# Performance work log

Hardware: AMD Instinct MI355X
Metric: run time of the kernel (lower is better)

## Reference

```python
import jax, jax.numpy as jnp
import numpy as np
import math

EMBED = 256
NH = 8            # num_heads
HD = EMBED // NH  # head_dim = 32
LEVELS = 4
P = 4             # points per level
SUMP = LEVELS * P # 16
OFFSET_SCALE = 0.5
SPATIAL = ((80, 80), (40, 40), (20, 20), (10, 10))  # (H, W) per level
BS, LQ = 4, 4096
LV = sum(h * w for h, w in SPATIAL)  # 8500


def _offset_bias():
    # replicates _reset_parameters grid init for sampling_offsets.bias
    thetas = np.arange(NH, dtype=np.float32) * (2.0 * math.pi / NH)
    grid = np.stack([np.cos(thetas), np.sin(thetas)], -1)  # [NH,2]
    grid = grid / np.abs(grid).max(-1, keepdims=True)
    grid = np.tile(grid.reshape(NH, 1, 2), (1, SUMP, 1))   # [NH,SUMP,2]
    scaling = np.concatenate([np.arange(1, P + 1) for _ in range(LEVELS)]).reshape(1, SUMP, 1)
    grid = grid * scaling
    return jnp.asarray(grid.reshape(-1), dtype=jnp.float32)  # [NH*SUMP*2]


def setup_inputs() -> dict:
    key = jax.random.key(0)
    ks = jax.random.split(key, 8)
    xavier = lambda k, fi, fo: jax.random.uniform(k, (fi, fo), jnp.float32,
                                                  -math.sqrt(6.0 / (fi + fo)), math.sqrt(6.0 / (fi + fo)))
    return {
        "query": jax.random.normal(ks[0], (BS, LQ, EMBED), jnp.float32),
        "reference_points": jax.random.uniform(ks[1], (BS, LQ, 1, 4), jnp.float32),
        "value": jax.random.normal(ks[2], (BS, LV, EMBED), jnp.float32),
        # sampling_offsets: weight is zero-init in torch; use small random so offsets depend on query
        "W_off": jax.random.normal(ks[3], (EMBED, NH * SUMP * 2), jnp.float32) * 0.01,
        "b_off": _offset_bias(),
        "W_attn": jax.random.normal(ks[4], (EMBED, NH * SUMP), jnp.float32) * 0.01,
        "b_attn": jnp.zeros((NH * SUMP,), jnp.float32),
        "W_v": xavier(ks[5], EMBED, EMBED),
        "b_v": jnp.zeros((EMBED,), jnp.float32),
        "W_o": xavier(ks[6], EMBED, EMBED),
        "b_o": jnp.zeros((EMBED,), jnp.float32),
    }


def _bilinear_sample(v_l, loc, Hl, Wl):
    """grid_sample (bilinear, zero padding, align_corners=False) on one level.
    v_l: [bs, NH, Hl*Wl, HD]; loc: [bs, Lq, NH, P, 2] in [0,1] (x=width, y=height).
    Returns [bs, Lq, NH, P, HD]."""
    bs, lq, nh, p, _ = loc.shape
    x = loc[..., 0] * Wl - 0.5
    y = loc[..., 1] * Hl - 0.5
    x0 = jnp.floor(x)
    y0 = jnp.floor(y)
    lx, ly = x - x0, y - y0
    x0i = x0.astype(jnp.int32)
    y0i = y0.astype(jnp.int32)

    def corner(xi, yi, w):
        valid = ((xi >= 0) & (xi < Wl) & (yi >= 0) & (yi < Hl)).astype(v_l.dtype)
        idx = jnp.clip(yi, 0, Hl - 1) * Wl + jnp.clip(xi, 0, Wl - 1)  # [bs,Lq,NH,P]
        idx = jnp.transpose(idx, (0, 2, 1, 3)).reshape(bs, nh, lq * p)
        g = jnp.take_along_axis(v_l, idx[..., None], axis=2)          # [bs,NH,Lq*P,HD]
        g = g.reshape(bs, nh, lq, p, HD).transpose(0, 2, 1, 3, 4)     # [bs,Lq,NH,P,HD]
        return g * (w * valid)[..., None]

    return (corner(x0i, y0i, (1 - lx) * (1 - ly))
            + corner(x0i + 1, y0i, lx * (1 - ly))
            + corner(x0i, y0i + 1, (1 - lx) * ly)
            + corner(x0i + 1, y0i + 1, lx * ly))


def reference(query, reference_points, value, W_off, b_off, W_attn, b_attn, W_v, b_v, W_o, b_o):
    bs, lq = query.shape[:2]
    lv = value.shape[1]

    v = (value @ W_v + b_v).reshape(bs, lv, NH, HD)

    off = (query @ W_off + b_off).reshape(bs, lq, NH, SUMP, 2)
    attn = jax.nn.softmax((query @ W_attn + b_attn).reshape(bs, lq, NH, SUMP), axis=-1)

    # reference_points last dim == 4 path (box refs)
    nps = jnp.full((SUMP, 1), 1.0 / P, dtype=query.dtype)  # num_points_scale
    loc = (reference_points[:, :, None, :, :2]
           + off * nps * reference_points[:, :, None, :, 2:] * OFFSET_SCALE)  # [bs,Lq,NH,SUMP,2]

    out = jnp.zeros((bs, lq, NH, HD), dtype=query.dtype)
    v_start, p_start = 0, 0
    for (Hl, Wl) in SPATIAL:
        n = Hl * Wl
        v_l = jnp.transpose(v[:, v_start:v_start + n], (0, 2, 1, 3))  # [bs,NH,n,HD]
        loc_l = loc[:, :, :, p_start:p_start + P]
        w_l = attn[:, :, :, p_start:p_start + P]
        sampled = _bilinear_sample(v_l, loc_l, Hl, Wl)                # [bs,Lq,NH,P,HD]
        out = out + jnp.einsum('blhpd,blhp->blhd', sampled, w_l)
        v_start += n
        p_start += P

    return out.reshape(bs, lq, EMBED) @ W_o + b_o
```

## Files before the change

### kernel.cpp

```cpp
#include <hip/hip_runtime.h>

#define NH 8
#define HD 32
#define SUMP 16
#define LQ 4096
#define BS 4
#define LV 8500
#define NQ (BS * LQ)
#define MV (BS * LV)

typedef float f32x4 __attribute__((ext_vector_type(4)));
typedef _Float16 f16x8 __attribute__((ext_vector_type(8)));

__global__ __launch_bounds__(256) void prep_kernel(
    const float* __restrict__ Wv, const float* __restrict__ Woff,
    const float* __restrict__ Wattn, const float* __restrict__ Wo,
    const float* __restrict__ boff, const float* __restrict__ battn,
    _Float16* __restrict__ WtVf, _Float16* __restrict__ WtOAf,
    _Float16* __restrict__ WtOf, float* __restrict__ biasOA)
{
    int g = blockIdx.x * 256 + threadIdx.x;
    int gl; _Float16* dst; int which;
    if (g < 65536)       { gl = g;          dst = WtVf;  which = 0; }
    else if (g < 163840) { gl = g - 65536;  dst = WtOAf; which = 1; }
    else                 { gl = g - 163840; dst = WtOf;  which = 2; }
    int e = gl & 7, m16 = (gl >> 3) & 15, q = (gl >> 7) & 3, C = (gl >> 9) & 7, T = gl >> 12;
    int n = T * 16 + m16, k = C * 32 + q * 8 + e;
    float w;
    if (which == 0)      w = Wv[k * 256 + n];
    else if (which == 1) w = (n < 256) ? Woff[k * 256 + n] : Wattn[k * 128 + (n - 256)];
    else                 w = Wo[k * 256 + n];
    dst[gl] = (_Float16)w;
    if (blockIdx.x == 0) biasOA[threadIdx.x] = boff[threadIdx.x];
    if (blockIdx.x == 1 && threadIdx.x < 128) biasOA[256 + threadIdx.x] = battn[threadIdx.x];
}

template <int NI, bool V_MODE, bool A_F16>
__device__ __forceinline__ void gemm_body(
    const float* __restrict__ A32, const _Float16* __restrict__ A16,
    const _Float16* __restrict__ Bf,
    const float* __restrict__ bias, void* __restrict__ Cv,
    int M, int N, int mb, int nb, _Float16* As )
{
    const int t = threadIdx.x;
    const int wave = t >> 6, lane = t & 63;
    const int quad = lane >> 4, l16 = lane & 15;
    const int mbase = mb * 128 + (wave & 1) * 64;
    const int ntile0 = nb * (2 * NI) + (wave >> 1) * NI;

    const int srow = t >> 2, skq = t & 3;
    int gm0 = mb * 128 + srow;        if (gm0 > M - 1) gm0 = M - 1;
    int gm1 = mb * 128 + srow + 64;   if (gm1 > M - 1) gm1 = M - 1;
    const float* ap0 = A32 ? A32 + (size_t)gm0 * 256 + skq * 8 : nullptr;
    const float* ap1 = A32 ? A32 + (size_t)gm1 * 256 + skq * 8 : nullptr;
    const _Float16* hp0 = A16 ? A16 + (size_t)gm0 * 256 + skq * 8 : nullptr;
    const _Float16* hp1 = A16 ? A16 + (size_t)gm1 * 256 + skq * 8 : nullptr;
    const int slot0 = (((srow >> 4)) * 64 + skq * 16 + ((srow & 15) ^ skq)) * 8;
    const int slot1 = ((((srow + 64) >> 4)) * 64 + skq * 16 + ((srow & 15) ^ skq)) * 8;

    const _Float16* bp[NI];
    #pragma unroll
    for (int ni = 0; ni < NI; ++ni)
        bp[ni] = Bf + (size_t)(ntile0 + ni) * 4096 + lane * 8;

    float a0[8], a1[8];
    f16x8 a0h, a1h;
    f16x8 bcur[NI], bnxt[NI];
    f32x4 acc[4][NI] = {};

    if (A_F16) {
        a0h = *(const f16x8*)(hp0);
        a1h = *(const f16x8*)(hp1);
    } else {
        *(float4*)(a0 + 0) = *(const float4*)(ap0 + 0);
        *(float4*)(a0 + 4) = *(const float4*)(ap0 + 4);
        *(float4*)(a1 + 0) = *(const float4*)(ap1 + 0);
        *(float4*)(a1 + 4) = *(const float4*)(ap1 + 4);
    }
    #pragma unroll
    for (int ni = 0; ni < NI; ++ni) bcur[ni] = *(const f16x8*)(bp[ni]);

    #pragma unroll
    for (int k = 0; k < 8; ++k) {
        _Float16* buf = As + (k & 1) * 4096;
        f16x8 c0, c1;
        if (A_F16) { c0 = a0h; c1 = a1h; }
        else {
            #pragma unroll
            for (int j = 0; j < 8; ++j) { c0[j] = (_Float16)a0[j]; c1[j] = (_Float16)a1[j]; }
        }
        *(f16x8*)(buf + slot0) = c0;
        *(f16x8*)(buf + slot1) = c1;
        __syncthreads();
        if (k < 7) {
            const int k0 = (k + 1) * 32;
            if (A_F16) {
                a0h = *(const f16x8*)(hp0 + k0);
                a1h = *(const f16x8*)(hp1 + k0);
            } else {
                *(float4*)(a0 + 0) = *(const float4*)(ap0 + k0);
                *(float4*)(a0 + 4) = *(const float4*)(ap0 + k0 + 4);
                *(float4*)(a1 + 0) = *(const float4*)(ap1 + k0);
                *(float4*)(a1 + 4) = *(const float4*)(ap1 + k0 + 4);
            }
            #pragma unroll
            for (int ni = 0; ni < NI; ++ni) bnxt[ni] = *(const f16x8*)(bp[ni] + (k + 1) * 512);
        }
        f16x8 af[4];
        #pragma unroll
        for (int mi = 0; mi < 4; ++mi)
            af[mi] = *(const f16x8*)(buf + (((wave & 1) * 4 + mi) * 64 + quad * 16 + (l16 ^ quad)) * 8);
        #pragma unroll
        for (int mi = 0; mi < 4; ++mi)
            #pragma unroll
            for (int ni = 0; ni < NI; ++ni)
                acc[mi][ni] = __builtin_amdgcn_mfma_f32_16x16x32_f16(af[mi], bcur[ni], acc[mi][ni], 0, 0, 0);
        #pragma unroll
        for (int ni = 0; ni < NI; ++ni) bcur[ni] = bnxt[ni];
    }

    if (V_MODE) {
        #pragma unroll
        for (int mi = 0; mi < 4; ++mi) {
            int mq = mbase + mi * 16 + quad * 4;
            size_t rb[4]; int vld[4];
            #pragma unroll
            for (int r = 0; r < 4; ++r) {
                int m = mq + r;
                vld[r] = (m < M);
                int b = m / LV; int pos = m - b * LV;
                rb[r] = ((size_t)b * NH * LV + pos) * 32;
            }
            #pragma unroll
            for (int ni = 0; ni < NI; ++ni) {
                int n = (ntile0 + ni) * 16 + l16;
                float bv = bias[n];
                int h = n >> 5, d = n & 31;
                size_t ho = (size_t)h * (LV * 32) + d;
                #pragma unroll
                for (int r = 0; r < 4; ++r)
                    if (vld[r]) ((_Float16*)Cv)[rb[r] + ho] = (_Float16)(acc[mi][ni][r] + bv);
            }
        }
    } else {
        #pragma unroll
        for (int ni = 0; ni < NI; ++ni) {
            int n = (ntile0 + ni) * 16 + l16;
            float bv = bias[n];
            #pragma unroll
            for (int mi = 0; mi < 4; ++mi) {
                int mq = mbase + mi * 16 + quad * 4;
                #pragma unroll
                for (int r = 0; r < 4; ++r)
                    ((float*)Cv)[(size_t)(mq + r) * N + n] = acc[mi][ni][r] + bv;
            }
        }
    }
}

__global__ __launch_bounds__(256) void gemm_dual_kernel(
    const float* __restrict__ value, const _Float16* __restrict__ WtVf,
    const float* __restrict__ b_v, _Float16* __restrict__ v_f16,
    const float* __restrict__ query, const _Float16* __restrict__ WtOAf,
    const float* __restrict__ biasOA, float* __restrict__ oa)
{
    __shared__ __align__(16) _Float16 As[2 * 4096];
    int bid = blockIdx.x;
    if (bid < 1064) {
        gemm_body<2, true, false>(value, nullptr, WtVf, b_v, v_f16, MV, 256,
                                  bid % 266, bid / 266, As);
    } else {
        int q = bid - 1064;
        gemm_body<2, false, false>(query, nullptr, WtOAf, biasOA, oa, NQ, 384,
                                   q % 128, q / 128, As);
    }
}

__global__ __launch_bounds__(256) void gemm_o_kernel(
    const _Float16* __restrict__ mid, const _Float16* __restrict__ WtOf,
    const float* __restrict__ b_o, float* __restrict__ out)
{
    __shared__ __align__(16) _Float16 As[2 * 4096];
    gemm_body<2, false, true>(nullptr, mid, WtOf, b_o, out, NQ, 256,
                              blockIdx.x & 127, blockIdx.x >> 7, As);
}

__global__ void sample_kernel(
    const _Float16* __restrict__ v,
    const float* __restrict__ oa,
    const float* __restrict__ refp,
    _Float16* __restrict__ mid)
{
    const int row0 = blockIdx.x * 2;
    const int t = threadIdx.x;
    const int wave = t >> 6, lane = t & 63;

    __shared__ __align__(16) char smem[8704];
    float*  s_lx  = (float*)smem;
    float*  s_ly  = (float*)(smem + 1024);
    float*  s_raw = (float*)(smem + 2048);
    int2*   s_pk  = (int2*)smem;
    float4* s_w4  = (float4*)(smem + 2176);
    float*  s_mx  = (float*)(smem + 6528);
    float*  s_is  = (float*)(smem + 6592);
    float*  s_part = (float*)(smem + 6656);

    {
        int q = t >> 7, e = t & 127;
        int row = row0 + q;
        float4 r4 = *(const float4*)(refp + (size_t)row * 4);
        float2 o2 = *(const float2*)(oa + (size_t)row * 384 + e * 2);
        s_lx[q * 128 + e]  = r4.x + o2.x * 0.125f * r4.z;
        s_ly[q * 128 + e]  = r4.y + o2.y * 0.125f * r4.w;
        s_raw[q * 128 + e] = oa[(size_t)row * 384 + 256 + e];
    }
    __syncthreads();
    if (t < 16) {
        int q = t >> 3, h = t & 7;
        float mx = -1e30f;
        #pragma unroll
        for (int p = 0; p < SUMP; ++p) mx = fmaxf(mx, s_raw[q * 128 + h * 16 + p]);
        float sm = 0.f;
        #pragma unroll
        for (int p = 0; p < SUMP; ++p) sm += __expf(s_raw[q * 128 + h * 16 + p] - mx);
        s_mx[t] = mx; s_is[t] = 1.f / sm;
    }
    __syncthreads();
    int2 r_pk;
    float4 r_w4;
    {
        int q = t >> 7, e = t & 127, h = e >> 4, p = e & 15, l = p >> 2;
        int Wl = 80 >> l;
        int vst = (l == 0) ? 0 : (l == 1) ? 6400 : (l == 2) ? 8000 : 8400;
        float w = __expf(s_raw[q * 128 + e] - s_mx[q * 8 + h]) * s_is[q * 8 + h];
        float x = s_lx[q * 128 + e] * Wl - 0.5f;
        float y = s_ly[q * 128 + e] * Wl - 0.5f;
        float x0f = floorf(x), y0f = floorf(y);
        float lx = x - x0f, ly = y - y0f;
        int x0 = (int)x0f, y0 = (int)y0f;
        int x1 = x0 + 1, y1 = y0 + 1;
        float mx0 = (x0 >= 0 && x0 < Wl) ? 1.f : 0.f;
        float mx1 = (x1 >= 0 && x1 < Wl) ? 1.f : 0.f;
        float my0 = (y0 >= 0 && y0 < Wl) ? 1.f : 0.f;
        float my1 = (y1 >= 0 && y1 < Wl) ? 1.f : 0.f;
        int cx0 = min(max(x0, 0), Wl - 1), cx1 = min(max(x1, 0), Wl - 1);
        int cy0 = min(max(y0, 0), Wl - 1), cy1 = min(max(y1, 0), Wl - 1);
        r_pk.x = (vst + cy0 * Wl + cx0) * 64;
        r_pk.y = ((cx1 - cx0) * 64) | (((cy1 - cy0) * Wl * 64) << 16);
        r_w4.x = w * (1.f - lx) * (1.f - ly) * mx0 * my0;
        r_w4.y = w * lx * (1.f - ly) * mx1 * my0;
        r_w4.z = w * (1.f - lx) * ly * mx0 * my1;
        r_w4.w = w * lx * ly * mx1 * my1;
    }
    __syncthreads();
    {
        int q = t >> 7, e = t & 127, h = e >> 4, p = e & 15;
        int s = (q * 8 + h) * 17 + p;
        s_pk[s] = r_pk; s_w4[s] = r_w4;
    }
    __syncthreads();
    {
        const int q = wave >> 1, wp = wave & 1;
        const int pgl = lane >> 5, hh = (lane >> 2) & 7, dv2 = lane & 3;
        const int row = row0 + q;
        const int b = row >> 12;
        const char* vb = (const char*)v + ((size_t)(b * NH + hh) * LV) * 64 + dv2 * 16;
        float acc8[8] = {};
        #pragma unroll
        for (int j = 0; j < 4; ++j) {
            int p = (wp * 2 + pgl) * 4 + j;
            int s = (q * 8 + hh) * 17 + p;
            int2 pk = s_pk[s];
            float4 w4 = s_w4[s];
            int dx = pk.y & 0xffff, dy = pk.y >> 16;
            f16x8 g00 = *(const f16x8*)(vb + pk.x);
            f16x8 g01 = *(const f16x8*)(vb + pk.x + dx);
            f16x8 g10 = *(const f16x8*)(vb + pk.x + dy);
            f16x8 g11 = *(const f16x8*)(vb + pk.x + dx + dy);
            #pragma unroll
            for (int c = 0; c < 8; ++c)
                acc8[c] += w4.x * (float)g00[c] + w4.y * (float)g01[c]
                         + w4.z * (float)g10[c] + w4.w * (float)g11[c];
        }
        #pragma unroll
        for (int c = 0; c < 8; ++c) acc8[c] += __shfl_xor(acc8[c], 32, 64);
        if (wp == 1 && lane < 32) {
            #pragma unroll
            for (int c = 0; c < 8; ++c) s_part[q * 256 + c * 32 + lane] = acc8[c];
        }
        __syncthreads();
        if (wp == 0 && lane < 32) {
            f16x8 m8;
            #pragma unroll
            for (int c = 0; c < 8; ++c)
                m8[c] = (_Float16)(acc8[c] + s_part[q * 256 + c * 32 + lane]);
            *(f16x8*)(mid + (size_t)row * 256 + hh * 32 + dv2 * 8) = m8;
        }
    }
}

extern "C" void kernel_launch(void* const* d_in, const int* in_sizes, int n_in,
                              void* d_out, int out_size, void* d_ws, size_t ws_size,
                              hipStream_t stream) {
    const float* query  = (const float*)d_in[0];
    const float* refp   = (const float*)d_in[1];
    const float* value  = (const float*)d_in[2];
    const float* W_off  = (const float*)d_in[3];
    const float* b_off  = (const float*)d_in[4];
    const float* W_attn = (const float*)d_in[5];
    const float* b_attn = (const float*)d_in[6];
    const float* W_v    = (const float*)d_in[7];
    const float* b_v    = (const float*)d_in[8];
    const float* W_o    = (const float*)d_in[9];
    const float* b_o    = (const float*)d_in[10];

    char* ws = (char*)d_ws;
    _Float16* v_f16  = (_Float16*)(ws + 0);
    float*    oa_f32 = (float*)(ws + 17408000);
    _Float16* mid    = (_Float16*)(ws + 42573824);
    _Float16* WtVf   = (_Float16*)(ws + 50962432);
    _Float16* WtOAf  = (_Float16*)(ws + 51093504);
    _Float16* WtOf   = (_Float16*)(ws + 51290112);
    float*    biasOA = (float*)(ws + 51421184);

    prep_kernel<<<896, 256, 0, stream>>>(W_v, W_off, W_attn, W_o, b_off, b_attn,
                                         WtVf, WtOAf, WtOf, biasOA);
    gemm_dual_kernel<<<1832, 256, 0, stream>>>(
        value, WtVf, b_v, v_f16, query, WtOAf, biasOA, oa_f32);
    sample_kernel<<<NQ / 2, 256, 0, stream>>>(v_f16, oa_f32, refp, mid);
    gemm_o_kernel<<<512, 256, 0, stream>>>(mid, WtOf, b_o, (float*)d_out);
}
```

Baseline: 183.4 us.

## Replace shared-memory block GEMM with independent per-wave register GEMM tiles

The block-cooperative GEMM, which staged A tiles through double-buffered LDS with __syncthreads, is replaced by a wave-level GEMM. Each wave loads its own 64x32 A fragments directly from global memory into registers and prefetches the next K slice. This removes LDS traffic and block barriers and adds an occupancy hint of 4 blocks per CU. In exchange, A rows are no longer shared across waves (each wave rereads A for its N tiles), and the per-lane row-strided global loads are less coalesced. The grid mapping assumes the launch counts stay unchanged.

```diff
diff --git a/kernel.cpp b/kernel.cpp
--- a/kernel.cpp
+++ b/kernel.cpp
@@ -35,105 +35,107 @@
     if (blockIdx.x == 1 && threadIdx.x < 128) biasOA[256 + threadIdx.x] = battn[threadIdx.x];
 }
 
-template <int NI, bool V_MODE, bool A_F16>
-__device__ __forceinline__ void gemm_body(
+__device__ __forceinline__ f16x8 cvt8(const float4& lo, const float4& hi) {
+    f16x8 r;
+    r[0] = (_Float16)lo.x; r[1] = (_Float16)lo.y; r[2] = (_Float16)lo.z; r[3] = (_Float16)lo.w;
+    r[4] = (_Float16)hi.x; r[5] = (_Float16)hi.y; r[6] = (_Float16)hi.z; r[7] = (_Float16)hi.w;
+    return r;
+}
+
+template <bool V_MODE, bool A_F16>
+__device__ __forceinline__ void wave_gemm(
     const float* __restrict__ A32, const _Float16* __restrict__ A16,
-    const _Float16* __restrict__ Bf,
-    const float* __restrict__ bias, void* __restrict__ Cv,
-    int M, int N, int mb, int nb, _Float16* As )
-{
-    const int t = threadIdx.x;
-    const int wave = t >> 6, lane = t & 63;
+    const _Float16* __restrict__ Bf, const float* __restrict__ bias,
+    void* __restrict__ Cv, int M, int N, int mt, int nt)
+{
+    const int lane = threadIdx.x & 63;
     const int quad = lane >> 4, l16 = lane & 15;
-    const int mbase = mb * 128 + (wave & 1) * 64;
-    const int ntile0 = nb * (2 * NI) + (wave >> 1) * NI;
-
-    const int srow = t >> 2, skq = t & 3;
-    int gm0 = mb * 128 + srow;        if (gm0 > M - 1) gm0 = M - 1;
-    int gm1 = mb * 128 + srow + 64;   if (gm1 > M - 1) gm1 = M - 1;
-    const float* ap0 = A32 ? A32 + (size_t)gm0 * 256 + skq * 8 : nullptr;
-    const float* ap1 = A32 ? A32 + (size_t)gm1 * 256 + skq * 8 : nullptr;
-    const _Float16* hp0 = A16 ? A16 + (size_t)gm0 * 256 + skq * 8 : nullptr;
-    const _Float16* hp1 = A16 ? A16 + (size_t)gm1 * 256 + skq * 8 : nullptr;
-    const int slot0 = (((srow >> 4)) * 64 + skq * 16 + ((srow & 15) ^ skq)) * 8;
-    const int slot1 = ((((srow + 64) >> 4)) * 64 + skq * 16 + ((srow & 15) ^ skq)) * 8;
-
-    const _Float16* bp[NI];
+
+    const _Float16* bp[2];
     #pragma unroll
-    for (int ni = 0; ni < NI; ++ni)
-        bp[ni] = Bf + (size_t)(ntile0 + ni) * 4096 + lane * 8;
-
-    float a0[8], a1[8];
-    f16x8 a0h, a1h;
-    f16x8 bcur[NI], bnxt[NI];
-    f32x4 acc[4][NI] = {};
+    for (int ni = 0; ni < 2; ++ni)
+        bp[ni] = Bf + (size_t)(nt * 2 + ni) * 4096 + lane * 8;
+
+    const float* ap[4];
+    const _Float16* hp[4];
+    #pragma unroll
+    for (int mi = 0; mi < 4; ++mi) {
+        int r = mt * 64 + mi * 16 + l16;
+        if (r > M - 1) r = M - 1;
+        if (A_F16) hp[mi] = A16 + (size_t)r * 256 + quad * 8;
+        else       ap[mi] = A32 + (size_t)r * 256 + quad * 8;
+    }
+
+    f32x4 acc[4][2] = {};
+    f16x8 aC[4], bC[2];
 
     if (A_F16) {
-        a0h = *(const f16x8*)(hp0);
-        a1h = *(const f16x8*)(hp1);
+        #pragma unroll
+        for (int mi = 0; mi < 4; ++mi) aC[mi] = *(const f16x8*)(hp[mi]);
     } else {
-        *(float4*)(a0 + 0) = *(const float4*)(ap0 + 0);
-        *(float4*)(a0 + 4) = *(const float4*)(ap0 + 4);
-        *(float4*)(a1 + 0) = *(const float4*)(ap1 + 0);
-        *(float4*)(a1 + 4) = *(const float4*)(ap1 + 4);
+        #pragma unroll
+        for (int mi = 0; mi < 4; ++mi) {
+            float4 lo = *(const float4*)(ap[mi] + 0);
+            float4 hi = *(const float4*)(ap[mi] + 4);
+            aC[mi] = cvt8(lo, hi);
+        }
     }
     #pragma unroll
-    for (int ni = 0; ni < NI; ++ni) bcur[ni] = *(const f16x8*)(bp[ni]);
+    for (int ni = 0; ni < 2; ++ni) bC[ni] = *(const f16x8*)(bp[ni]);
 
     #pragma unroll
     for (int k = 0; k < 8; ++k) {
-        _Float16* buf = As + (k & 1) * 4096;
-        f16x8 c0, c1;
-        if (A_F16) { c0 = a0h; c1 = a1h; }
-        else {
-            #pragma unroll
-            for (int j = 0; j < 8; ++j) { c0[j] = (_Float16)a0[j]; c1[j] = (_Float16)a1[j]; }
-        }
-        *(f16x8*)(buf + slot0) = c0;
-        *(f16x8*)(buf + slot1) = c1;
-        __syncthreads();
+        float4 anL[4], anH[4];
+        f16x8 ahN[4], bN[2];
         if (k < 7) {
             const int k0 = (k + 1) * 32;
             if (A_F16) {
-                a0h = *(const f16x8*)(hp0 + k0);
-                a1h = *(const f16x8*)(hp1 + k0);
+                #pragma unroll
+                for (int mi = 0; mi < 4; ++mi) ahN[mi] = *(const f16x8*)(hp[mi] + k0);
             } else {
-                *(float4*)(a0 + 0) = *(const float4*)(ap0 + k0);
-                *(float4*)(a0 + 4) = *(const float4*)(ap0 + k0 + 4);
-                *(float4*)(a1 + 0) = *(const float4*)(ap1 + k0);
-                *(float4*)(a1 + 4) = *(const float4*)(ap1 + k0 + 4);
-            }
-            #pragma unroll
-            for (int ni = 0; ni < NI; ++ni) bnxt[ni] = *(const f16x8*)(bp[ni] + (k + 1) * 512);
-        }
-        f16x8 af[4];
+                #pragma unroll
+                for (int mi = 0; mi < 4; ++mi) {
+                    anL[mi] = *(const float4*)(ap[mi] + k0);
+                    anH[mi] = *(const float4*)(ap[mi] + k0 + 4);
+                }
+            }
+            #pragma unroll
+            for (int ni = 0; ni < 2; ++ni) bN[ni] = *(const f16x8*)(bp[ni] + (k + 1) * 512);
+        }
         #pragma unroll
         for (int mi = 0; mi < 4; ++mi)
-            af[mi] = *(const f16x8*)(buf + (((wave & 1) * 4 + mi) * 64 + quad * 16 + (l16 ^ quad)) * 8);
-        #pragma unroll
-        for (int mi = 0; mi < 4; ++mi)
-            #pragma unroll
-            for (int ni = 0; ni < NI; ++ni)
-                acc[mi][ni] = __builtin_amdgcn_mfma_f32_16x16x32_f16(af[mi], bcur[ni], acc[mi][ni], 0, 0, 0);
-        #pragma unroll
-        for (int ni = 0; ni < NI; ++ni) bcur[ni] = bnxt[ni];
+            #pragma unroll
+            for (int ni = 0; ni < 2; ++ni)
+                acc[mi][ni] = __builtin_amdgcn_mfma_f32_16x16x32_f16(aC[mi], bC[ni], acc[mi][ni], 0, 0, 0);
+        if (k < 7) {
+            if (A_F16) {
+                #pragma unroll
+                for (int mi = 0; mi < 4; ++mi) aC[mi] = ahN[mi];
+            } else {
+                #pragma unroll
+                for (int mi = 0; mi < 4; ++mi) aC[mi] = cvt8(anL[mi], anH[mi]);
+            }
+            #pragma unroll
+            for (int ni = 0; ni < 2; ++ni) bC[ni] = bN[ni];
+        }
     }
 
     if (V_MODE) {
         #pragma unroll
         for (int mi = 0; mi < 4; ++mi) {
-            int mq = mbase + mi * 16 + quad * 4;
+            int mq = mt * 64 + mi * 16 + quad * 4;
             size_t rb[4]; int vld[4];
             #pragma unroll
             for (int r = 0; r < 4; ++r) {
                 int m = mq + r;
                 vld[r] = (m < M);
-                int b = m / LV; int pos = m - b * LV;
+                int mm = vld[r] ? m : 0;
+                int b = mm / LV; int pos = mm - b * LV;
                 rb[r] = ((size_t)b * NH * LV + pos) * 32;
             }
             #pragma unroll
-            for (int ni = 0; ni < NI; ++ni) {
-                int n = (ntile0 + ni) * 16 + l16;
+            for (int ni = 0; ni < 2; ++ni) {
+                int n = (nt * 2 + ni) * 16 + l16;
                 float bv = bias[n];
                 int h = n >> 5, d = n & 31;
                 size_t ho = (size_t)h * (LV * 32) + d;
@@ -144,12 +146,12 @@
         }
     } else {
         #pragma unroll
-        for (int ni = 0; ni < NI; ++ni) {
-            int n = (ntile0 + ni) * 16 + l16;
+        for (int ni = 0; ni < 2; ++ni) {
+            int n = (nt * 2 + ni) * 16 + l16;
             float bv = bias[n];
             #pragma unroll
             for (int mi = 0; mi < 4; ++mi) {
-                int mq = mbase + mi * 16 + quad * 4;
+                int mq = mt * 64 + mi * 16 + quad * 4;
                 #pragma unroll
                 for (int r = 0; r < 4; ++r)
                     ((float*)Cv)[(size_t)(mq + r) * N + n] = acc[mi][ni][r] + bv;
@@ -158,31 +160,33 @@
     }
 }
 
-__global__ __launch_bounds__(256) void gemm_dual_kernel(
+__global__ __launch_bounds__(256, 4) void gemm_dual_kernel(
     const float* __restrict__ value, const _Float16* __restrict__ WtVf,
     const float* __restrict__ b_v, _Float16* __restrict__ v_f16,
     const float* __restrict__ query, const _Float16* __restrict__ WtOAf,
     const float* __restrict__ biasOA, float* __restrict__ oa)
 {
-    __shared__ __align__(16) _Float16 As[2 * 4096];
     int bid = blockIdx.x;
+    int wave = threadIdx.x >> 6;
     if (bid < 1064) {
-        gemm_body<2, true, false>(value, nullptr, WtVf, b_v, v_f16, MV, 256,
-                                  bid % 266, bid / 266, As);
+        int g = bid * 4 + wave;
+        wave_gemm<true, false>(value, nullptr, WtVf, b_v, v_f16, MV, 256,
+                               g >> 3, g & 7);
     } else {
-        int q = bid - 1064;
-        gemm_body<2, false, false>(query, nullptr, WtOAf, biasOA, oa, NQ, 384,
-                                   q % 128, q / 128, As);
-    }
-}
-
-__global__ __launch_bounds__(256) void gemm_o_kernel(
+        int g = (bid - 1064) * 4 + wave;
+        int mt = g / 12;
+        wave_gemm<false, false>(query, nullptr, WtOAf, biasOA, oa, NQ, 384,
+                                mt, g - mt * 12);
+    }
+}
+
+__global__ __launch_bounds__(256, 4) void gemm_o_kernel(
     const _Float16* __restrict__ mid, const _Float16* __restrict__ WtOf,
     const float* __restrict__ b_o, float* __restrict__ out)
 {
-    __shared__ __align__(16) _Float16 As[2 * 4096];
-    gemm_body<2, false, true>(nullptr, mid, WtOf, b_o, out, NQ, 256,
-                              blockIdx.x & 127, blockIdx.x >> 7, As);
+    int g = blockIdx.x * 4 + (threadIdx.x >> 6);
+    wave_gemm<false, true>(nullptr, mid, WtOf, b_o, out, NQ, 256,
+                           g >> 3, g & 7);
 }
 
 __global__ void sample_kernel(
```

Result: slower. 228.2 us (+24.4%).

## Restructure GEMMs to load full-K A row chunks into LDS once

Applied to the files above, without the earlier changes.

Each GEMM block now loads a 64-row by full-K (256) A tile into LDS once, with an XOR swizzle, before a single barrier, replacing the per-K-step double-buffered A staging with a barrier every step. Waves now split the N dimension: each wave covers 4 or 3 n-tiles (full N for the value and out projections, half of it for the fused offset/attention projection), so A is read from global memory fewer times across blocks and grid sizes shrink. This removes seven per-iteration barriers, at the cost of 32 KB of LDS per block, more registers for the large upfront loads, and fewer blocks in flight.

```diff
diff --git a/kernel.cpp b/kernel.cpp
--- a/kernel.cpp
+++ b/kernel.cpp
@@ -35,100 +35,99 @@
     if (blockIdx.x == 1 && threadIdx.x < 128) biasOA[256 + threadIdx.x] = battn[threadIdx.x];
 }
 
+__device__ __forceinline__ f16x8 cvt8(const float4& lo, const float4& hi) {
+    f16x8 r;
+    r[0] = (_Float16)lo.x; r[1] = (_Float16)lo.y; r[2] = (_Float16)lo.z; r[3] = (_Float16)lo.w;
+    r[4] = (_Float16)hi.x; r[5] = (_Float16)hi.y; r[6] = (_Float16)hi.z; r[7] = (_Float16)hi.w;
+    return r;
+}
+
 template <int NI, bool V_MODE, bool A_F16>
-__device__ __forceinline__ void gemm_body(
+__device__ __forceinline__ void chunk_gemm(
     const float* __restrict__ A32, const _Float16* __restrict__ A16,
-    const _Float16* __restrict__ Bf,
-    const float* __restrict__ bias, void* __restrict__ Cv,
-    int M, int N, int mb, int nb, _Float16* As )
+    const _Float16* __restrict__ Bf, const float* __restrict__ bias,
+    void* __restrict__ Cv, int M, int N, int mchunk, int ntbase,
+    _Float16* __restrict__ As )
 {
     const int t = threadIdx.x;
     const int wave = t >> 6, lane = t & 63;
     const int quad = lane >> 4, l16 = lane & 15;
-    const int mbase = mb * 128 + (wave & 1) * 64;
-    const int ntile0 = nb * (2 * NI) + (wave >> 1) * NI;
-
-    const int srow = t >> 2, skq = t & 3;
-    int gm0 = mb * 128 + srow;        if (gm0 > M - 1) gm0 = M - 1;
-    int gm1 = mb * 128 + srow + 64;   if (gm1 > M - 1) gm1 = M - 1;
-    const float* ap0 = A32 ? A32 + (size_t)gm0 * 256 + skq * 8 : nullptr;
-    const float* ap1 = A32 ? A32 + (size_t)gm1 * 256 + skq * 8 : nullptr;
-    const _Float16* hp0 = A16 ? A16 + (size_t)gm0 * 256 + skq * 8 : nullptr;
-    const _Float16* hp1 = A16 ? A16 + (size_t)gm1 * 256 + skq * 8 : nullptr;
-    const int slot0 = (((srow >> 4)) * 64 + skq * 16 + ((srow & 15) ^ skq)) * 8;
-    const int slot1 = ((((srow + 64) >> 4)) * 64 + skq * 16 + ((srow & 15) ^ skq)) * 8;
-
+
+    {
+        const int srow = t >> 2, schunk = t & 3;
+        int gr = mchunk * 64 + srow;
+        if (gr > M - 1) gr = M - 1;
+        if (A_F16) {
+            const _Float16* src = A16 + (size_t)gr * 256 + schunk * 64;
+            f16x8 hb[8];
+            #pragma unroll
+            for (int j = 0; j < 8; ++j) hb[j] = *(const f16x8*)(src + j * 8);
+            #pragma unroll
+            for (int j = 0; j < 8; ++j) {
+                int slot = (schunk * 8 + j) ^ (srow & 7);
+                *(f16x8*)(As + srow * 256 + slot * 8) = hb[j];
+            }
+        } else {
+            const float* src = A32 + (size_t)gr * 256 + schunk * 64;
+            float4 buf[16];
+            #pragma unroll
+            for (int j = 0; j < 16; ++j) buf[j] = *(const float4*)(src + j * 4);
+            #pragma unroll
+            for (int j = 0; j < 8; ++j) {
+                f16x8 h = cvt8(buf[2 * j], buf[2 * j + 1]);
+                int slot = (schunk * 8 + j) ^ (srow & 7);
+                *(f16x8*)(As + srow * 256 + slot * 8) = h;
+            }
+        }
+    }
+    __syncthreads();
+
+    const int ntile0 = ntbase + wave * NI;
     const _Float16* bp[NI];
     #pragma unroll
     for (int ni = 0; ni < NI; ++ni)
         bp[ni] = Bf + (size_t)(ntile0 + ni) * 4096 + lane * 8;
 
-    float a0[8], a1[8];
-    f16x8 a0h, a1h;
     f16x8 bcur[NI], bnxt[NI];
     f32x4 acc[4][NI] = {};
-
-    if (A_F16) {
-        a0h = *(const f16x8*)(hp0);
-        a1h = *(const f16x8*)(hp1);
-    } else {
-        *(float4*)(a0 + 0) = *(const float4*)(ap0 + 0);
-        *(float4*)(a0 + 4) = *(const float4*)(ap0 + 4);
-        *(float4*)(a1 + 0) = *(const float4*)(ap1 + 0);
-        *(float4*)(a1 + 4) = *(const float4*)(ap1 + 4);
-    }
     #pragma unroll
     for (int ni = 0; ni < NI; ++ni) bcur[ni] = *(const f16x8*)(bp[ni]);
 
     #pragma unroll
     for (int k = 0; k < 8; ++k) {
-        _Float16* buf = As + (k & 1) * 4096;
-        f16x8 c0, c1;
-        if (A_F16) { c0 = a0h; c1 = a1h; }
-        else {
-            #pragma unroll
-            for (int j = 0; j < 8; ++j) { c0[j] = (_Float16)a0[j]; c1[j] = (_Float16)a1[j]; }
-        }
-        *(f16x8*)(buf + slot0) = c0;
-        *(f16x8*)(buf + slot1) = c1;
-        __syncthreads();
         if (k < 7) {
-            const int k0 = (k + 1) * 32;
-            if (A_F16) {
-                a0h = *(const f16x8*)(hp0 + k0);
-                a1h = *(const f16x8*)(hp1 + k0);
-            } else {
-                *(float4*)(a0 + 0) = *(const float4*)(ap0 + k0);
-                *(float4*)(a0 + 4) = *(const float4*)(ap0 + k0 + 4);
-                *(float4*)(a1 + 0) = *(const float4*)(ap1 + k0);
-                *(float4*)(a1 + 4) = *(const float4*)(ap1 + k0 + 4);
-            }
             #pragma unroll
             for (int ni = 0; ni < NI; ++ni) bnxt[ni] = *(const f16x8*)(bp[ni] + (k + 1) * 512);
         }
         f16x8 af[4];
         #pragma unroll
-        for (int mi = 0; mi < 4; ++mi)
-            af[mi] = *(const f16x8*)(buf + (((wave & 1) * 4 + mi) * 64 + quad * 16 + (l16 ^ quad)) * 8);
+        for (int mi = 0; mi < 4; ++mi) {
+            int row = mi * 16 + l16;
+            int slot = (quad + k * 4) ^ (row & 7);
+            af[mi] = *(const f16x8*)(As + row * 256 + slot * 8);
+        }
         #pragma unroll
         for (int mi = 0; mi < 4; ++mi)
             #pragma unroll
             for (int ni = 0; ni < NI; ++ni)
                 acc[mi][ni] = __builtin_amdgcn_mfma_f32_16x16x32_f16(af[mi], bcur[ni], acc[mi][ni], 0, 0, 0);
-        #pragma unroll
-        for (int ni = 0; ni < NI; ++ni) bcur[ni] = bnxt[ni];
+        if (k < 7) {
+            #pragma unroll
+            for (int ni = 0; ni < NI; ++ni) bcur[ni] = bnxt[ni];
+        }
     }
 
     if (V_MODE) {
         #pragma unroll
         for (int mi = 0; mi < 4; ++mi) {
-            int mq = mbase + mi * 16 + quad * 4;
+            int mq = mchunk * 64 + mi * 16 + quad * 4;
             size_t rb[4]; int vld[4];
             #pragma unroll
             for (int r = 0; r < 4; ++r) {
                 int m = mq + r;
                 vld[r] = (m < M);
-                int b = m / LV; int pos = m - b * LV;
+                int mm = vld[r] ? m : 0;
+                int b = mm / LV; int pos = mm - b * LV;
                 rb[r] = ((size_t)b * NH * LV + pos) * 32;
             }
             #pragma unroll
@@ -149,7 +148,7 @@
             float bv = bias[n];
             #pragma unroll
             for (int mi = 0; mi < 4; ++mi) {
-                int mq = mbase + mi * 16 + quad * 4;
+                int mq = mchunk * 64 + mi * 16 + quad * 4;
                 #pragma unroll
                 for (int r = 0; r < 4; ++r)
                     ((float*)Cv)[(size_t)(mq + r) * N + n] = acc[mi][ni][r] + bv;
@@ -164,15 +163,15 @@
     const float* __restrict__ query, const _Float16* __restrict__ WtOAf,
     const float* __restrict__ biasOA, float* __restrict__ oa)
 {
-    __shared__ __align__(16) _Float16 As[2 * 4096];
+    __shared__ __align__(16) _Float16 As[64 * 256];
     int bid = blockIdx.x;
-    if (bid < 1064) {
-        gemm_body<2, true, false>(value, nullptr, WtVf, b_v, v_f16, MV, 256,
-                                  bid % 266, bid / 266, As);
+    if (bid < 532) {
+        chunk_gemm<4, true, false>(value, nullptr, WtVf, b_v, v_f16, MV, 256,
+                                   bid, 0, As);
     } else {
-        int q = bid - 1064;
-        gemm_body<2, false, false>(query, nullptr, WtOAf, biasOA, oa, NQ, 384,
-                                   q % 128, q / 128, As);
+        int g = bid - 532;
+        chunk_gemm<3, false, false>(query, nullptr, WtOAf, biasOA, oa, NQ, 384,
+                                    g >> 1, (g & 1) * 12, As);
     }
 }
 
@@ -180,9 +179,9 @@
     const _Float16* __restrict__ mid, const _Float16* __restrict__ WtOf,
     const float* __restrict__ b_o, float* __restrict__ out)
 {
-    __shared__ __align__(16) _Float16 As[2 * 4096];
-    gemm_body<2, false, true>(nullptr, mid, WtOf, b_o, out, NQ, 256,
-                              blockIdx.x & 127, blockIdx.x >> 7, As);
+    __shared__ __align__(16) _Float16 As[64 * 256];
+    chunk_gemm<4, false, true>(nullptr, mid, WtOf, b_o, out, NQ, 256,
+                               blockIdx.x, 0, As);
 }
 
 __global__ void sample_kernel(
@@ -325,8 +324,8 @@
 
     prep_kernel<<<896, 256, 0, stream>>>(W_v, W_off, W_attn, W_o, b_off, b_attn,
                                          WtVf, WtOAf, WtOf, biasOA);
-    gemm_dual_kernel<<<1832, 256, 0, stream>>>(
+    gemm_dual_kernel<<<1044, 256, 0, stream>>>(
         value, WtVf, b_v, v_f16, query, WtOAf, biasOA, oa_f32);
     sample_kernel<<<NQ / 2, 256, 0, stream>>>(v_f16, oa_f32, refp, mid);
-    gemm_o_kernel<<<512, 256, 0, stream>>>(mid, WtOf, b_o, (float*)d_out);
-}
+    gemm_o_kernel<<<256, 256, 0, stream>>>(mid, WtOf, b_o, (float*)d_out);
+}
```

Measured after the change: 174.3 us. 5.0% less time.
